# Kernel tuning notes

Measured on AMD Instinct MI355X. Metric: run time of the kernel, lower is better.

Reference implementation:

```python
import jax, jax.numpy as jnp
import numpy as np

N_NODES = 40000
N_EDGES = 400000
N_GRAPHS = 256
F_IN = 128
COND = 100
HEADS = 32
DIMS = [90, 45, 15, 5]
EPS = 1e-5


def setup_inputs() -> dict:
    key = jax.random.key(0)
    ks = iter(jax.random.split(key, 64))
    inp = {}
    inp["x"] = jax.random.normal(next(ks), (N_NODES, F_IN), dtype=jnp.float32)
    inp["edge_index"] = jax.random.randint(next(ks), (2, N_EDGES), 0, N_NODES, dtype=jnp.int32)
    inp["batch"] = jnp.sort(jax.random.randint(next(ks), (N_NODES,), 0, N_GRAPHS, dtype=jnp.int32))
    inp["conditional_features"] = jax.random.normal(next(ks), (COND,), dtype=jnp.float32)
    # GATConv params: W [in, H*C], a_src/a_dst [H, C], bias [C] (concat=False -> out is C)
    dims_in = [F_IN] + DIMS[:-1]
    for i, (ci, co) in enumerate(zip(dims_in, DIMS), start=1):
        sw = 1.0 / np.sqrt(ci)
        inp[f"W{i}"] = jax.random.normal(next(ks), (ci, HEADS * co), dtype=jnp.float32) * sw
        inp[f"as{i}"] = jax.random.normal(next(ks), (HEADS, co), dtype=jnp.float32) * (1.0 / np.sqrt(co))
        inp[f"ad{i}"] = jax.random.normal(next(ks), (HEADS, co), dtype=jnp.float32) * (1.0 / np.sqrt(co))
        inp[f"b{i}"] = jnp.zeros((co,), dtype=jnp.float32)
    # BatchNorm affine params (init gamma=1, beta=0) for sizes F_IN,90,45,15,5
    for i, c in enumerate([F_IN] + DIMS, start=1):
        inp[f"g{i}"] = jnp.ones((c,), dtype=jnp.float32)
        inp[f"be{i}"] = jnp.zeros((c,), dtype=jnp.float32)
    inp["fcW"] = jax.random.normal(next(ks), (DIMS[-1] + COND, 1), dtype=jnp.float32) * (1.0 / np.sqrt(DIMS[-1] + COND))
    inp["fcb"] = jnp.zeros((1,), dtype=jnp.float32)
    return inp


def _bn(x, g, b):
    # training-mode BatchNorm1d: batch statistics (biased var), eps=1e-5
    mu = x.mean(0)
    var = x.var(0)
    return g * (x - mu) * jax.lax.rsqrt(var + EPS) + b


def _gat(x, W, a_s, a_d, b, src, dst, n):
    H, C = a_s.shape
    h = (x @ W).reshape(n, H, C)                      # [N,H,C]
    s_src = jnp.einsum("nhc,hc->nh", h, a_s)
    s_dst = jnp.einsum("nhc,hc->nh", h, a_d)
    logit = jax.nn.leaky_relu(s_src[src] + s_dst[dst], 0.2)  # [E,H]
    m = jax.ops.segment_max(logit, dst, num_segments=n)
    e = jnp.exp(logit - m[dst])
    denom = jax.ops.segment_sum(e, dst, num_segments=n)
    alpha = e / denom[dst]                            # per-dst softmax, [E,H]
    out = jnp.zeros((n, C), dtype=x.dtype)
    for hi in range(H):  # fixed small loop over heads keeps peak memory at [E,C]
        out = out + jax.ops.segment_sum(alpha[:, hi, None] * h[src, hi, :], dst, num_segments=n)
    return out / H + b   # concat=False -> mean over heads, then bias


def reference(x, edge_index, batch, conditional_features,
              W1, as1, ad1, b1, W2, as2, ad2, b2, W3, as3, ad3, b3, W4, as4, ad4, b4,
              g1, be1, g2, be2, g3, be3, g4, be4, g5, be5, fcW, fcb):
    n = x.shape[0]
    loop = jnp.arange(n, dtype=edge_index.dtype)      # PyG GATConv adds self-loops by default
    src = jnp.concatenate([edge_index[0], loop])
    dst = jnp.concatenate([edge_index[1], loop])

    h = _bn(x, g1, be1)
    h = jax.nn.leaky_relu(_gat(h, W1, as1, ad1, b1, src, dst, n), 0.01)
    h = _bn(h, g2, be2)
    h = jax.nn.leaky_relu(_gat(h, W2, as2, ad2, b2, src, dst, n), 0.01)
    h = _bn(h, g3, be3)
    h = jax.nn.leaky_relu(_gat(h, W3, as3, ad3, b3, src, dst, n), 0.01)
    h = _bn(h, g4, be4)
    h = jax.nn.leaky_relu(_gat(h, W4, as4, ad4, b4, src, dst, n), 0.01)
    # dropout is identity in eval mode

    counts = jax.ops.segment_sum(jnp.ones((n,), dtype=h.dtype), batch, num_segments=N_GRAPHS)
    pooled = jax.ops.segment_sum(h, batch, num_segments=N_GRAPHS) / jnp.maximum(counts, 1.0)[:, None]
    z = jnp.concatenate([pooled, jnp.broadcast_to(conditional_features, (N_GRAPHS, COND))], axis=1)
    return jax.nn.sigmoid(z @ fcW + fcb).reshape(-1, 1)
```

## Files before the change

### kernel.cpp

```cpp
#include <hip/hip_runtime.h>
#include <hip/hip_bf16.h>

constexpr int NN = 40000;
constexpr int NE = 400000;
constexpr int NSLAB = 20000;
constexpr int MPAD = 20096;
constexpr int SCB = 256;
constexpr int SCHUNK = (NN + SCB - 1) / SCB;
constexpr int NPB = 512;

__device__ __forceinline__ unsigned short f2bf(float f) {
    unsigned int u = __float_as_uint(f);
    unsigned int r = (u + 0x7FFFu + ((u >> 16) & 1u)) >> 16;
    return (unsigned short)r;
}

__device__ __forceinline__ unsigned int cvt_pk_bf16(float a, float b) {
    unsigned int r;
    asm("v_cvt_pk_bf16_f32 %0, %1, %2" : "=v"(r) : "v"(a), "v"(b));
    return r;
}

__device__ __forceinline__ void load_lds16(const unsigned short* g, unsigned short* l) {
    __builtin_amdgcn_global_load_lds(
        (const __attribute__((address_space(1))) unsigned int*)(g),
        (__attribute__((address_space(3))) unsigned int*)(l), 16, 0, 0);
}

typedef __attribute__((ext_vector_type(8))) short bf16x8;
typedef __attribute__((ext_vector_type(4))) float f32x4;
typedef __attribute__((ext_vector_type(2))) float floatx2;

__global__ void bn_partial(const float* __restrict__ x, int N, int C,
                           float* __restrict__ partial) {
    int ch = threadIdx.x;
    if (ch >= C) return;
    float s = 0.f, sq = 0.f;
    for (int n = blockIdx.x; n < N; n += gridDim.x) {
        float v = x[(size_t)n * C + ch];
        s += v; sq += v * v;
    }
    partial[(size_t)blockIdx.x * 2 * C + ch]     = s;
    partial[(size_t)blockIdx.x * 2 * C + C + ch] = sq;
}

template <int CIN, int CP>
__global__ __launch_bounds__(256) void bn_apply_f(const float* __restrict__ x,
                                                  const float* __restrict__ partial,
                                                  const float* __restrict__ g,
                                                  const float* __restrict__ be,
                                                  float* __restrict__ scale_g,
                                                  float* __restrict__ shift_g,
                                                  unsigned short* __restrict__ xbn) {
    __shared__ float hs[2][128], hq[2][128];
    __shared__ float sc_l[CP], sh_l[CP];
    const int tid = threadIdx.x;
    const int half = tid >> 7, ch = tid & 127;
    if (ch < CIN) {
        float s = 0.f, sq = 0.f;
        for (int b = half * (NPB / 2); b < (half + 1) * (NPB / 2); ++b) {
            s  += partial[(size_t)b * 2 * CIN + ch];
            sq += partial[(size_t)b * 2 * CIN + CIN + ch];
        }
        hs[half][ch] = s; hq[half][ch] = sq;
    }
    __syncthreads();
    if (tid < CP) {
        float sc = 0.f, sh = 0.f;
        if (tid < CIN) {
            float s  = hs[0][tid] + hs[1][tid];
            float sq = hq[0][tid] + hq[1][tid];
            float mean = s / (float)NN;
            float var  = sq / (float)NN - mean * mean;
            float inv  = rsqrtf(var + 1e-5f);
            sc = g[tid] * inv;
            sh = be[tid] - mean * sc;
            if (blockIdx.x == 0) { scale_g[tid] = sc; shift_g[tid] = sh; }
        }
        sc_l[tid] = sc; sh_l[tid] = sh;
    }
    __syncthreads();
    const int total = NN * (CP / 2);
    for (int idx = blockIdx.x * 256 + tid; idx < total; idx += 256 * gridDim.x) {
        int n = idx / (CP / 2), c2 = idx % (CP / 2);
        int c = 2 * c2;
        float v0 = 0.f, v1 = 0.f;
        if (c < CIN)     v0 = sc_l[c] * x[(size_t)n * CIN + c] + sh_l[c];
        if (c + 1 < CIN) v1 = sc_l[c + 1] * x[(size_t)n * CIN + c + 1] + sh_l[c + 1];
        reinterpret_cast<unsigned int*>(xbn)[idx] = cvt_pk_bf16(v0, v1);
    }
}

struct PrepLayer {
    const float* W; const float* as_; const float* ad_;
    float* Wf; unsigned short* Wft; unsigned short* Wt;
    int CIN, CP, COUT, NP, bbase;
};
struct PrepArgs { PrepLayer L[4]; int nb; };

__global__ void prep_all(PrepArgs A) {
    int bid = blockIdx.x;
    int li = 0;
#pragma unroll
    for (int i = 1; i < 4; ++i)
        if (bid >= A.L[i].bbase) li = i;
    const PrepLayer& P = A.L[li];
    const int CIN = P.CIN, CP = P.CP, COUT = P.COUT;
    int b = bid - P.bbase;
    int tid = threadIdx.x;
    if (b < CP) {
        int cin = b;
        if (tid < 64) {
            int j = tid, h = j & 31;
            float s = 0.f;
            if (cin < CIN) {
                const float* a = (j < 32) ? P.as_ : P.ad_;
                const float* wrow = P.W + (size_t)cin * 32 * COUT + (size_t)h * COUT;
                const float* arow = a + (size_t)h * COUT;
                for (int c = 0; c < COUT; ++c) s += wrow[c] * arow[c];
            }
            P.Wf[cin * 64 + j] = s;
            P.Wft[j * CP + cin] = f2bf(s);
        }
    } else {
        int c = b - CP;
        for (int kk = tid; kk < 32 * CP; kk += blockDim.x) {
            int h = kk / CP, k = kk % CP;
            float v = 0.f;
            if (k < CIN && c < COUT)
                v = P.W[(size_t)k * (32 * COUT) + h * COUT + c] * (1.f / 32.f);
            P.Wt[(size_t)c * (32 * CP) + kk] = f2bf(v);
        }
    }
}

template <int CPK>
__global__ __launch_bounds__(256) void gemm_s(const unsigned short* __restrict__ xbn,
                                              const unsigned short* __restrict__ Wft,
                                              float* __restrict__ Sbuf) {
    constexpr int NC = CPK / 32;
    __shared__ unsigned short Ab[64 * 32];
    __shared__ unsigned short Bb[64 * 32];
    const int m0 = blockIdx.x * 64;
    const int tid = threadIdx.x;
    const int wv = tid >> 6, lane = tid & 63;
    const int mm = lane & 15, quad = lane >> 4;
    f32x4 acc[4];
#pragma unroll
    for (int t = 0; t < 4; ++t) acc[t] = f32x4{0.f, 0.f, 0.f, 0.f};

    for (int c = 0; c < NC; ++c) {
        int row = tid >> 2, gc = tid & 3;
        load_lds16(xbn + (size_t)(m0 + row) * CPK + c * 32 + gc * 8, Ab + (size_t)tid * 8);
        load_lds16(Wft + (size_t)row * CPK + c * 32 + gc * 8, Bb + (size_t)tid * 8);
        asm volatile("s_waitcnt vmcnt(0)" ::: "memory");
        __syncthreads();
        bf16x8 a = *reinterpret_cast<const bf16x8*>(&Ab[(wv * 16 + mm) * 32 + quad * 8]);
#pragma unroll
        for (int t = 0; t < 4; ++t) {
            bf16x8 b = *reinterpret_cast<const bf16x8*>(&Bb[(t * 16 + mm) * 32 + quad * 8]);
            acc[t] = __builtin_amdgcn_mfma_f32_16x16x32_bf16(a, b, acc[t], 0, 0, 0);
        }
        __syncthreads();
    }
    int rbase = m0 + wv * 16 + quad * 4;
#pragma unroll
    for (int t = 0; t < 4; ++t)
#pragma unroll
        for (int r = 0; r < 4; ++r)
            Sbuf[(size_t)(rbase + r) * 64 + t * 16 + mm] = acc[t][r];
}

__global__ __launch_bounds__(256) void gemm_bn(const float* __restrict__ X,
                                               const float* __restrict__ W,
                                               const float* __restrict__ scale,
                                               const float* __restrict__ shift,
                                               int Cin, int HC, float* __restrict__ OUT) {
    __shared__ float As[8][64];
    __shared__ float Bs[8][64];
    int tid = threadIdx.x;
    int n0 = blockIdx.y * 64;
    int j0 = blockIdx.x * 64;
    int tr = tid >> 4, tc = tid & 15;
    float acc[4][4] = {};
    for (int k0 = 0; k0 < Cin; k0 += 8) {
        int idx = tid;
#pragma unroll
        for (int it = 0; it < 2; ++it, idx += 256) {
            int row = idx >> 3, kk = idx & 7;
            int k = k0 + kk;
            float v = 0.f;
            if (k < Cin) v = scale[k] * X[(size_t)(n0 + row) * Cin + k] + shift[k];
            As[kk][row] = v;
        }
        int idx2 = tid;
#pragma unroll
        for (int it = 0; it < 2; ++it, idx2 += 256) {
            int col = idx2 & 63, kr = idx2 >> 6;
            int k = k0 + kr, j = j0 + col;
            float v = 0.f;
            if (k < Cin && j < HC) v = W[(size_t)k * HC + j];
            Bs[kr][col] = v;
        }
        __syncthreads();
#pragma unroll
        for (int kk = 0; kk < 8; ++kk) {
            float a[4], b[4];
#pragma unroll
            for (int i = 0; i < 4; ++i) a[i] = As[kk][tr * 4 + i];
#pragma unroll
            for (int j = 0; j < 4; ++j) b[j] = Bs[kk][tc * 4 + j];
#pragma unroll
            for (int i = 0; i < 4; ++i)
#pragma unroll
                for (int j = 0; j < 4; ++j) acc[i][j] += a[i] * b[j];
        }
        __syncthreads();
    }
#pragma unroll
    for (int i = 0; i < 4; ++i) {
        int row = n0 + tr * 4 + i;
#pragma unroll
        for (int j = 0; j < 4; ++j) {
            int col = j0 + tc * 4 + j;
            if (col < HC) OUT[(size_t)row * HC + col] = acc[i][j];
        }
    }
}

__global__ void deg_init(int* __restrict__ deg) {
    int n = blockIdx.x * blockDim.x + threadIdx.x;
    if (n < NN) deg[n] = 1;
}
__global__ void count_kernel(const int* __restrict__ dst, int* __restrict__ deg) {
    int e = blockIdx.x * blockDim.x + threadIdx.x;
    if (e < NE) atomicAdd(&deg[dst[e]], 1);
}
__global__ void scan_pass1(const int* __restrict__ deg, int* __restrict__ bsum) {
    __shared__ int red[256];
    int b = blockIdx.x, t = threadIdx.x;
    int lo = b * SCHUNK, hi = min(lo + SCHUNK, NN);
    int s = 0;
    for (int i = lo + t; i < hi; i += 256) s += deg[i];
    red[t] = s;
    __syncthreads();
    for (int off = 128; off > 0; off >>= 1) {
        if (t < off) red[t] += red[t + off];
        __syncthreads();
    }
    if (t == 0) bsum[b] = red[0];
}
__global__ void scan_pass2(const int* __restrict__ bsum, int* __restrict__ boff,
                           int* __restrict__ rowptr) {
    __shared__ int lds[256];
    int t = threadIdx.x;
    int v0 = bsum[t];
    lds[t] = v0;
    __syncthreads();
    for (int off = 1; off < 256; off <<= 1) {
        int v = (t >= off) ? lds[t - off] : 0;
        __syncthreads();
        lds[t] += v;
        __syncthreads();
    }
    boff[t] = lds[t] - v0;
    if (t == 255) rowptr[NN] = lds[255];
}
__global__ void scan_pass3(const int* __restrict__ deg, const int* __restrict__ boff,
                           int* __restrict__ rowptr, int* __restrict__ cursor) {
    __shared__ int lds[256];
    int b = blockIdx.x, t = threadIdx.x;
    int i = b * SCHUNK + t;
    int d = (t < SCHUNK && i < NN) ? deg[i] : 0;
    lds[t] = d;
    __syncthreads();
    for (int off = 1; off < 256; off <<= 1) {
        int v = (t >= off) ? lds[t - off] : 0;
        __syncthreads();
        lds[t] += v;
        __syncthreads();
    }
    if (t < SCHUNK && i < NN) {
        int excl = lds[t] - d + boff[b];
        rowptr[i] = excl;
        cursor[i] = excl;
    }
}
__global__ void scatter_all(const int* __restrict__ src, const int* __restrict__ dst,
                            int* __restrict__ cursor, int* __restrict__ colsrc) {
    int e = blockIdx.x * blockDim.x + threadIdx.x;
    if (e < NE) {
        int pos = atomicAdd(&cursor[dst[e]], 1);
        colsrc[pos] = src[e];
    } else if (e < NE + NN) {
        int n = e - NE;
        int pos = atomicAdd(&cursor[n], 1);
        colsrc[pos] = n;
    }
}

template <int CIN, int CP>
__global__ __launch_bounds__(256) void agg_x(const unsigned short* __restrict__ xbn,
                                             const float* __restrict__ S,
                                             const int* __restrict__ rowptr,
                                             const int* __restrict__ colsrc,
                                             int n0, unsigned short* __restrict__ z) {
    constexpr int BS = 256, CH = 32, J = CP / 8;
    constexpr bool V4 = (J % 4 == 0);
    constexpr int NACC = V4 ? (J / 4) : (J / 2);
    __shared__ __align__(16) float x_lds[CH * CP];
    __shared__ float w_lds[CH * 32];
    __shared__ int cs_lds[CH];
    __shared__ float red_m[8][32];
    __shared__ float red_s[8][32];

    int n = n0 + blockIdx.x;
    int tid = threadIdx.x;
    int start = rowptr[n], end = rowptr[n + 1];
    const int h = tid & 31, g = tid >> 5;
    const int cbase = g * J;
    const float sd = S[(size_t)n * 64 + 32 + h];

    float m_reg = -INFINITY, d_reg = 0.f;
    f32x4 acc4[V4 ? NACC : 1];
    floatx2 acc2[V4 ? 1 : NACC];
    if constexpr (V4) {
#pragma unroll
        for (int j = 0; j < NACC; ++j) acc4[j] = f32x4{0.f, 0.f, 0.f, 0.f};
    } else {
#pragma unroll
        for (int j = 0; j < NACC; ++j) acc2[j] = floatx2{0.f, 0.f};
    }

    for (int chunk = start; chunk < end; chunk += CH) {
        int ce = min(CH, end - chunk);
        int ce32 = ce * 32;
        if (tid < 32 && tid < ce) cs_lds[tid] = colsrc[chunk + tid];
        __syncthreads();

        float lreg[4];
        float pmx = -INFINITY;
#pragma unroll
        for (int p = 0; p < 4; ++p) {
            int idx = p * 256 + tid;
            lreg[p] = -INFINITY;
            if (idx < ce32) {
                int e = idx >> 5;
                float l = S[(size_t)cs_lds[e] * 64 + h] + sd;
                l = l > 0.f ? l : 0.2f * l;
                lreg[p] = l;
                pmx = fmaxf(pmx, l);
            }
        }
        red_m[g][h] = pmx;
        for (int idx = tid; idx < ce * (CP / 4); idx += BS) {
            int e = idx / (CP / 4), c4 = idx % (CP / 4);
            uint2 u = reinterpret_cast<const uint2*>(xbn)[(size_t)cs_lds[e] * (CP / 4) + c4];
            f32x4 t;
            t[0] = __uint_as_float(u.x << 16);
            t[1] = __uint_as_float(u.x & 0xFFFF0000u);
            t[2] = __uint_as_float(u.y << 16);
            t[3] = __uint_as_float(u.y & 0xFFFF0000u);
            *reinterpret_cast<f32x4*>(&x_lds[e * CP + 4 * c4]) = t;
        }
        __syncthreads();

        float cm = red_m[0][h];
#pragma unroll
        for (int s2 = 1; s2 < 8; ++s2) cm = fmaxf(cm, red_m[s2][h]);
        float newm = fmaxf(m_reg, cm);
        float r = (m_reg == -INFINITY) ? 0.f : __expf(m_reg - newm);
        m_reg = newm;

        float ps = 0.f;
#pragma unroll
        for (int p = 0; p < 4; ++p) {
            int idx = p * 256 + tid;
            if (idx < ce32) {
                float v = __expf(lreg[p] - m_reg);
                w_lds[idx] = v;
                ps += v;
            }
        }
        red_s[g][h] = ps;
        __syncthreads();

        float ss = red_s[0][h];
#pragma unroll
        for (int s2 = 1; s2 < 8; ++s2) ss += red_s[s2][h];
        d_reg = d_reg * r + ss;

        if constexpr (V4) {
            f32x4 rr4 = {r, r, r, r};
#pragma unroll
            for (int j = 0; j < NACC; ++j) acc4[j] *= rr4;
            for (int e = 0; e < ce; ++e) {
                float w = w_lds[e * 32 + h];
                f32x4 w4 = {w, w, w, w};
                const f32x4* xv = reinterpret_cast<const f32x4*>(&x_lds[e * CP + cbase]);
#pragma unroll
                for (int j = 0; j < NACC; ++j) acc4[j] += w4 * xv[j];
            }
        } else {
            floatx2 rr2 = {r, r};
#pragma unroll
            for (int j = 0; j < NACC; ++j) acc2[j] *= rr2;
            for (int e = 0; e < ce; ++e) {
                float w = w_lds[e * 32 + h];
                floatx2 w2 = {w, w};
                const floatx2* xv = reinterpret_cast<const floatx2*>(&x_lds[e * CP + cbase]);
#pragma unroll
                for (int j = 0; j < NACC; ++j) acc2[j] += w2 * xv[j];
            }
        }
    }

    float dinv = 1.f / d_reg;
    if constexpr (V4) {
        uint2* zp = reinterpret_cast<uint2*>(
            z + (size_t)(n - n0) * (32 * CP) + h * CP + cbase);
#pragma unroll
        for (int j = 0; j < NACC; ++j) {
            uint2 t;
            t.x = cvt_pk_bf16(acc4[j][0] * dinv, acc4[j][1] * dinv);
            t.y = cvt_pk_bf16(acc4[j][2] * dinv, acc4[j][3] * dinv);
            zp[j] = t;
        }
    } else {
        unsigned int* zp = reinterpret_cast<unsigned int*>(
            z + (size_t)(n - n0) * (32 * CP) + h * CP + cbase);
#pragma unroll
        for (int j = 0; j < NACC; ++j)
            zp[j] = cvt_pk_bf16(acc2[j][0] * dinv, acc2[j][1] * dinv);
    }
}

template <int NT, int KP, int KS, bool FB>
__global__ __launch_bounds__(256) void gemm_z_t(const unsigned short* __restrict__ z,
                                                const unsigned short* __restrict__ Wt,
                                                float* __restrict__ obuf,
                                                const float* __restrict__ bias,
                                                int n0, int COUT) {
    constexpr int NP = NT * 16;
    constexpr int KSEG = KP / KS;
    constexpr int NC = KSEG / 64;
    constexpr int MT = 128;
    __shared__ unsigned short Abuf[2][MT * 64];
    __shared__ unsigned short Bbuf[2][NP * 64];

    const int m0 = blockIdx.x * MT;
    const int kbeg = blockIdx.y * KSEG;
    const int tid = threadIdx.x;
    const int wv = tid >> 6;
    const int lane = tid & 63;
    const int mm = lane & 15, quad = lane >> 4;

    auto stage = [&](int buf, int kk) {
#pragma unroll
        for (int it = 0; it < 4; ++it) {
            int gi = it * 256 + tid;
            int row = gi >> 3, gc = gi & 7;
            int srow = m0 + row;
            if (srow > NSLAB - 1) srow = NSLAB - 1;
            const unsigned short* src = z + (size_t)srow * KP + kk + gc * 8;
            unsigned short* dst = &Abuf[buf][(size_t)(it * 256 + wv * 64) * 8];
            load_lds16(src, dst);
        }
#pragma unroll
        for (int it = 0; it < (NP * 8 + 255) / 256; ++it) {
            int gi = it * 256 + tid;
            if (gi < NP * 8) {
                int row = gi >> 3, gc = gi & 7;
                const unsigned short* src = Wt + (size_t)row * KP + kk + gc * 8;
                unsigned short* dst = &Bbuf[buf][(size_t)(it * 256 + wv * 64) * 8];
                load_lds16(src, dst);
            }
        }
    };

    f32x4 acc[2][NT];
#pragma unroll
    for (int f = 0; f < 2; ++f)
#pragma unroll
        for (int t = 0; t < NT; ++t) acc[f][t] = f32x4{0.f, 0.f, 0.f, 0.f};

    stage(0, kbeg);
    for (int c = 0; c < NC; ++c) {
        asm volatile("s_waitcnt vmcnt(0)" ::: "memory");
        __syncthreads();
        int cur = c & 1;
        if (c + 1 < NC) stage(cur ^ 1, kbeg + (c + 1) * 64);
        const unsigned short* Ab = Abuf[cur];
        const unsigned short* Bb = Bbuf[cur];
#pragma unroll
        for (int hh = 0; hh < 2; ++hh) {
            bf16x8 a0 = *reinterpret_cast<const bf16x8*>(&Ab[(wv * 32 + mm) * 64 + hh * 32 + quad * 8]);
            bf16x8 a1 = *reinterpret_cast<const bf16x8*>(&Ab[(wv * 32 + 16 + mm) * 64 + hh * 32 + quad * 8]);
#pragma unroll
            for (int t = 0; t < NT; ++t) {
                bf16x8 b = *reinterpret_cast<const bf16x8*>(&Bb[(t * 16 + mm) * 64 + hh * 32 + quad * 8]);
                acc[0][t] = __builtin_amdgcn_mfma_f32_16x16x32_bf16(a0, b, acc[0][t], 0, 0, 0);
                acc[1][t] = __builtin_amdgcn_mfma_f32_16x16x32_bf16(a1, b, acc[1][t], 0, 0, 0);
            }
        }
        __syncthreads();
    }

    int row0 = quad * 4;
    if constexpr (FB) {
#pragma unroll
        for (int f = 0; f < 2; ++f) {
#pragma unroll
            for (int t = 0; t < NT; ++t) {
                int cc = t * 16 + mm;
#pragma unroll
                for (int r = 0; r < 4; ++r) {
                    int m = m0 + wv * 32 + f * 16 + row0 + r;
                    if (m < NSLAB && cc < COUT) {
                        float v = acc[f][t][r] + bias[cc];
                        v = v > 0.f ? v : 0.01f * v;
                        obuf[(size_t)(n0 + m) * COUT + cc] = v;
                    }
                }
            }
        }
    } else {
        float* pb = obuf + (size_t)blockIdx.y * MPAD * NP;
#pragma unroll
        for (int f = 0; f < 2; ++f) {
#pragma unroll
            for (int t = 0; t < NT; ++t) {
                int cc = t * 16 + mm;
#pragma unroll
                for (int r = 0; r < 4; ++r) {
                    int m = m0 + wv * 32 + f * 16 + row0 + r;
                    pb[(size_t)m * NP + cc] = acc[f][t][r];
                }
            }
        }
    }
}

__global__ void reduce_parts(const float* __restrict__ pbuf, int KS, int NPAD, int COUT,
                             const float* __restrict__ bias, int n0,
                             float* __restrict__ xout) {
    int idx = blockIdx.x * blockDim.x + threadIdx.x;
    if (idx >= NSLAB * NPAD) return;
    int m = idx / NPAD, c = idx % NPAD;
    if (c >= COUT) return;
    float s = 0.f;
    for (int p = 0; p < KS; ++p) s += pbuf[(size_t)p * MPAD * NPAD + (size_t)m * NPAD + c];
    float v = s + bias[c];
    v = v > 0.f ? v : 0.01f * v;
    xout[(size_t)(n0 + m) * COUT + c] = v;
}

__global__ __launch_bounds__(64) void pool_head(const float* __restrict__ x4,
                                                const int* __restrict__ batch,
                                                const float* __restrict__ cond,
                                                const float* __restrict__ fcW,
                                                const float* __restrict__ fcb,
                                                float* __restrict__ out) {
    int g = blockIdx.x;
    int lane = threadIdx.x;
    int lo = 0, hi = NN;
    while (lo < hi) { int mid = (lo + hi) >> 1; if (batch[mid] < g) lo = mid + 1; else hi = mid; }
    int lo2 = lo, hi2 = NN;
    while (lo2 < hi2) { int mid = (lo2 + hi2) >> 1; if (batch[mid] < g + 1) lo2 = mid + 1; else hi2 = mid; }
    int beg = lo, end = lo2;

    float s[5] = {0.f, 0.f, 0.f, 0.f, 0.f};
    for (int n = beg + lane; n < end; n += 64) {
#pragma unroll
        for (int c = 0; c < 5; ++c) s[c] += x4[(size_t)n * 5 + c];
    }
    float cz = 0.f;
    if (lane < 100) cz = cond[lane] * fcW[5 + lane];
    if (lane + 64 < 100) cz += cond[lane + 64] * fcW[5 + lane + 64];
#pragma unroll
    for (int off = 32; off > 0; off >>= 1) {
#pragma unroll
        for (int c = 0; c < 5; ++c) s[c] += __shfl_down(s[c], off, 64);
        cz += __shfl_down(cz, off, 64);
    }
    if (lane == 0) {
        float cnt = fmaxf((float)(end - beg), 1.f);
        float zv = fcb[0] + cz;
#pragma unroll
        for (int c = 0; c < 5; ++c) zv += (s[c] / cnt) * fcW[c];
        out[g] = 1.f / (1.f + __expf(-zv));
    }
}

struct LayerBufs {
    float* partial; float* scale; float* shift;
    unsigned short* xbn; unsigned short* zbuf;
    float* Sbuf; float* pbuf; const int* rowptr; const int* colsrc;
};

template <int CIN, int CP, int COUT, int NP, int NT, int KS>
static void run_layer(const float* xin, const float* Wf, const unsigned short* Wft,
                      const unsigned short* Wt,
                      const float* Bv, const float* G, const float* Be,
                      float* xout, const LayerBufs& B, hipStream_t stream) {
    constexpr int KP = 32 * CP;
    constexpr int NPAD = NT * 16;
    bn_partial<<<NPB, 128, 0, stream>>>(xin, NN, CIN, B.partial);
    bn_apply_f<CIN, CP><<<512, 256, 0, stream>>>(xin, B.partial, G, Be,
                                                 B.scale, B.shift, B.xbn);
    if constexpr (CP >= 64) {
        gemm_s<CP><<<NN / 64, 256, 0, stream>>>(B.xbn, Wft, B.Sbuf);
    } else {
        gemm_bn<<<dim3(1, NN / 64), 256, 0, stream>>>(xin, Wf, B.scale, B.shift, CIN, 64, B.Sbuf);
    }
    for (int s = 0; s < 2; ++s) {
        int n0 = s * NSLAB;
        agg_x<CIN, CP><<<NSLAB, 256, 0, stream>>>(B.xbn, B.Sbuf, B.rowptr, B.colsrc, n0, B.zbuf);
        if constexpr (KS > 1) {
            gemm_z_t<NT, KP, KS, false><<<dim3(MPAD / 128, KS), 256, 0, stream>>>(
                B.zbuf, Wt, B.pbuf, nullptr, n0, COUT);
            reduce_parts<<<(NSLAB * NPAD + 255) / 256, 256, 0, stream>>>(
                B.pbuf, KS, NPAD, COUT, Bv, n0, xout);
        } else {
            gemm_z_t<NT, KP, 1, true><<<dim3(MPAD / 128, 1), 256, 0, stream>>>(
                B.zbuf, Wt, xout, Bv, n0, COUT);
        }
    }
}

extern "C" void kernel_launch(void* const* d_in, const int* in_sizes, int n_in,
                              void* d_out, int out_size, void* d_ws, size_t ws_size,
                              hipStream_t stream) {
    (void)in_sizes; (void)n_in; (void)out_size;
    const float* x     = (const float*)d_in[0];
    const int*   ei    = (const int*)d_in[1];
    const int*   batch = (const int*)d_in[2];
    const float* cond  = (const float*)d_in[3];
    const float* W[4]  = {(const float*)d_in[4],  (const float*)d_in[8],
                          (const float*)d_in[12], (const float*)d_in[16]};
    const float* Asp[4] = {(const float*)d_in[5],  (const float*)d_in[9],
                           (const float*)d_in[13], (const float*)d_in[17]};
    const float* Adp[4] = {(const float*)d_in[6],  (const float*)d_in[10],
                           (const float*)d_in[14], (const float*)d_in[18]};
    const float* Bv[4]  = {(const float*)d_in[7],  (const float*)d_in[11],
                           (const float*)d_in[15], (const float*)d_in[19]};
    const float* G[4]   = {(const float*)d_in[20], (const float*)d_in[22],
                           (const float*)d_in[24], (const float*)d_in[26]};
    const float* Be[4]  = {(const float*)d_in[21], (const float*)d_in[23],
                           (const float*)d_in[25], (const float*)d_in[27]};
    const float* fcW = (const float*)d_in[30];
    const float* fcb = (const float*)d_in[31];
    float* out = (float*)d_out;

    char* base = (char*)d_ws;
    size_t off = 0;
    auto alloc = [&](size_t b) {
        size_t o = off;
        off += (b + 255) & ~(size_t)255;
        return (void*)(base + o);
    };
    unsigned short* zbuf = (unsigned short*)alloc((size_t)NSLAB * 4096 * 2);
    unsigned short* xbn  = (unsigned short*)alloc((size_t)NN * 128 * 2);
    float* pbuf    = (float*)alloc((size_t)4 * MPAD * 96 * 4);
    float* xbuf    = (float*)alloc((size_t)NN * 90 * 4);
    float* Sbuf    = (float*)alloc((size_t)NN * 64 * 4);
    float* partial = (float*)alloc((size_t)NPB * 2 * 128 * 4);
    float* scale   = (float*)alloc(128 * 4);
    float* shift   = (float*)alloc(128 * 4);
    const int CPs[4]  = {128, 96, 48, 16};
    const int NPs[4]  = {96, 48, 16, 16};
    const int CINs[4] = {128, 90, 45, 15};
    const int COUTs[4] = {90, 45, 15, 5};
    float* Wf_a[4]; unsigned short* Wft_a[4]; unsigned short* Wt_a[4];
    for (int i = 0; i < 4; ++i) {
        Wf_a[i]  = (float*)alloc((size_t)CPs[i] * 64 * 4);
        Wft_a[i] = (unsigned short*)alloc((size_t)64 * CPs[i] * 2);
        Wt_a[i]  = (unsigned short*)alloc((size_t)NPs[i] * 32 * CPs[i] * 2);
    }
    int* deg     = (int*)alloc((size_t)NN * 4);
    int* rowptr  = (int*)alloc((size_t)(NN + 1) * 4);
    int* cursor  = (int*)alloc((size_t)NN * 4);
    int* colsrc  = (int*)alloc((size_t)(NE + NN) * 4);
    int* bsum    = (int*)alloc((size_t)SCB * 4);
    int* boff    = (int*)alloc((size_t)SCB * 4);
    if (off > ws_size) return;

    const int* srcp = ei;
    const int* dstp = ei + NE;

    PrepArgs PA;
    int bb = 0;
    for (int i = 0; i < 4; ++i) {
        PA.L[i] = PrepLayer{W[i], Asp[i], Adp[i], Wf_a[i], Wft_a[i], Wt_a[i],
                            CINs[i], CPs[i], COUTs[i], NPs[i], bb};
        bb += CPs[i] + NPs[i];
    }
    PA.nb = bb;
    prep_all<<<bb, 256, 0, stream>>>(PA);

    deg_init<<<(NN + 255) / 256, 256, 0, stream>>>(deg);
    count_kernel<<<(NE + 255) / 256, 256, 0, stream>>>(dstp, deg);
    scan_pass1<<<SCB, 256, 0, stream>>>(deg, bsum);
    scan_pass2<<<1, 256, 0, stream>>>(bsum, boff, rowptr);
    scan_pass3<<<SCB, 256, 0, stream>>>(deg, boff, rowptr, cursor);
    scatter_all<<<(NE + NN + 255) / 256, 256, 0, stream>>>(srcp, dstp, cursor, colsrc);

    LayerBufs B{partial, scale, shift, xbn, zbuf, Sbuf, pbuf, rowptr, colsrc};

    run_layer<128, 128, 90, 96, 6, 4>(x,    Wf_a[0], Wft_a[0], Wt_a[0], Bv[0], G[0], Be[0], xbuf, B, stream);
    run_layer< 90,  96, 45, 48, 3, 3>(xbuf, Wf_a[1], Wft_a[1], Wt_a[1], Bv[1], G[1], Be[1], xbuf, B, stream);
    run_layer< 45,  48, 15, 16, 1, 1>(xbuf, Wf_a[2], Wft_a[2], Wt_a[2], Bv[2], G[2], Be[2], xbuf, B, stream);
    run_layer< 15,  16,  5, 16, 1, 1>(xbuf, Wf_a[3], Wft_a[3], Wt_a[3], Bv[3], G[3], Be[3], xbuf, B, stream);

    pool_head<<<256, 64, 0, stream>>>(xbuf, batch, cond, fcW, fcb, out);
}
```

Before: 1.043 ms.

## Shrink aggregation chunk and GEMM M-tile, replace degree init with memset

The edge chunk in agg_x drops from 32 to 16, which halves the LDS footprint and register arrays. That should let more blocks fit per CU, though it adds more chunk iterations and syncs for high-degree nodes. The z-GEMM M tile drops from 128 to 64 rows, so each wave handles one 16-row fragment and twice as many blocks launch, giving more parallelism at the cost of less reuse of the B tile. The deg_init kernel is replaced by hipMemsetAsync, and the self-loop +1 is folded into the scan passes.

```diff
diff --git a/kernel.cpp b/kernel.cpp
--- a/kernel.cpp
+++ b/kernel.cpp
@@ -228,10 +228,6 @@
     }
 }
 
-__global__ void deg_init(int* __restrict__ deg) {
-    int n = blockIdx.x * blockDim.x + threadIdx.x;
-    if (n < NN) deg[n] = 1;
-}
 __global__ void count_kernel(const int* __restrict__ dst, int* __restrict__ deg) {
     int e = blockIdx.x * blockDim.x + threadIdx.x;
     if (e < NE) atomicAdd(&deg[dst[e]], 1);
@@ -241,7 +237,7 @@
     int b = blockIdx.x, t = threadIdx.x;
     int lo = b * SCHUNK, hi = min(lo + SCHUNK, NN);
     int s = 0;
-    for (int i = lo + t; i < hi; i += 256) s += deg[i];
+    for (int i = lo + t; i < hi; i += 256) s += deg[i] + 1;
     red[t] = s;
     __syncthreads();
     for (int off = 128; off > 0; off >>= 1) {
@@ -271,7 +267,7 @@
     __shared__ int lds[256];
     int b = blockIdx.x, t = threadIdx.x;
     int i = b * SCHUNK + t;
-    int d = (t < SCHUNK && i < NN) ? deg[i] : 0;
+    int d = (t < SCHUNK && i < NN) ? (deg[i] + 1) : 0;
     lds[t] = d;
     __syncthreads();
     for (int off = 1; off < 256; off <<= 1) {
@@ -305,9 +301,10 @@
                                              const int* __restrict__ rowptr,
                                              const int* __restrict__ colsrc,
                                              int n0, unsigned short* __restrict__ z) {
-    constexpr int BS = 256, CH = 32, J = CP / 8;
+    constexpr int BS = 256, CH = 16, J = CP / 8;
     constexpr bool V4 = (J % 4 == 0);
     constexpr int NACC = V4 ? (J / 4) : (J / 2);
+    constexpr int LIT = CH * 32 / 256;
     __shared__ __align__(16) float x_lds[CH * CP];
     __shared__ float w_lds[CH * 32];
     __shared__ int cs_lds[CH];
@@ -335,13 +332,13 @@
     for (int chunk = start; chunk < end; chunk += CH) {
         int ce = min(CH, end - chunk);
         int ce32 = ce * 32;
-        if (tid < 32 && tid < ce) cs_lds[tid] = colsrc[chunk + tid];
-        __syncthreads();
-
-        float lreg[4];
+        if (tid < CH && tid < ce) cs_lds[tid] = colsrc[chunk + tid];
+        __syncthreads();
+
+        float lreg[LIT];
         float pmx = -INFINITY;
 #pragma unroll
-        for (int p = 0; p < 4; ++p) {
+        for (int p = 0; p < LIT; ++p) {
             int idx = p * 256 + tid;
             lreg[p] = -INFINITY;
             if (idx < ce32) {
@@ -374,7 +371,7 @@
 
         float ps = 0.f;
 #pragma unroll
-        for (int p = 0; p < 4; ++p) {
+        for (int p = 0; p < LIT; ++p) {
             int idx = p * 256 + tid;
             if (idx < ce32) {
                 float v = __expf(lreg[p] - m_reg);
@@ -444,7 +441,7 @@
     constexpr int NP = NT * 16;
     constexpr int KSEG = KP / KS;
     constexpr int NC = KSEG / 64;
-    constexpr int MT = 128;
+    constexpr int MT = 64;
     __shared__ unsigned short Abuf[2][MT * 64];
     __shared__ unsigned short Bbuf[2][NP * 64];
 
@@ -457,7 +454,7 @@
 
     auto stage = [&](int buf, int kk) {
 #pragma unroll
-        for (int it = 0; it < 4; ++it) {
+        for (int it = 0; it < 2; ++it) {
             int gi = it * 256 + tid;
             int row = gi >> 3, gc = gi & 7;
             int srow = m0 + row;
@@ -478,11 +475,9 @@
         }
     };
 
-    f32x4 acc[2][NT];
-#pragma unroll
-    for (int f = 0; f < 2; ++f)
-#pragma unroll
-        for (int t = 0; t < NT; ++t) acc[f][t] = f32x4{0.f, 0.f, 0.f, 0.f};
+    f32x4 acc[NT];
+#pragma unroll
+    for (int t = 0; t < NT; ++t) acc[t] = f32x4{0.f, 0.f, 0.f, 0.f};
 
     stage(0, kbeg);
     for (int c = 0; c < NC; ++c) {
@@ -494,13 +489,11 @@
         const unsigned short* Bb = Bbuf[cur];
 #pragma unroll
         for (int hh = 0; hh < 2; ++hh) {
-            bf16x8 a0 = *reinterpret_cast<const bf16x8*>(&Ab[(wv * 32 + mm) * 64 + hh * 32 + quad * 8]);
-            bf16x8 a1 = *reinterpret_cast<const bf16x8*>(&Ab[(wv * 32 + 16 + mm) * 64 + hh * 32 + quad * 8]);
+            bf16x8 a0 = *reinterpret_cast<const bf16x8*>(&Ab[(wv * 16 + mm) * 64 + hh * 32 + quad * 8]);
 #pragma unroll
             for (int t = 0; t < NT; ++t) {
                 bf16x8 b = *reinterpret_cast<const bf16x8*>(&Bb[(t * 16 + mm) * 64 + hh * 32 + quad * 8]);
-                acc[0][t] = __builtin_amdgcn_mfma_f32_16x16x32_bf16(a0, b, acc[0][t], 0, 0, 0);
-                acc[1][t] = __builtin_amdgcn_mfma_f32_16x16x32_bf16(a1, b, acc[1][t], 0, 0, 0);
+                acc[t] = __builtin_amdgcn_mfma_f32_16x16x32_bf16(a0, b, acc[t], 0, 0, 0);
             }
         }
         __syncthreads();
@@ -509,33 +502,27 @@
     int row0 = quad * 4;
     if constexpr (FB) {
 #pragma unroll
-        for (int f = 0; f < 2; ++f) {
-#pragma unroll
-            for (int t = 0; t < NT; ++t) {
-                int cc = t * 16 + mm;
-#pragma unroll
-                for (int r = 0; r < 4; ++r) {
-                    int m = m0 + wv * 32 + f * 16 + row0 + r;
-                    if (m < NSLAB && cc < COUT) {
-                        float v = acc[f][t][r] + bias[cc];
-                        v = v > 0.f ? v : 0.01f * v;
-                        obuf[(size_t)(n0 + m) * COUT + cc] = v;
-                    }
+        for (int t = 0; t < NT; ++t) {
+            int cc = t * 16 + mm;
+#pragma unroll
+            for (int r = 0; r < 4; ++r) {
+                int m = m0 + wv * 16 + row0 + r;
+                if (m < NSLAB && cc < COUT) {
+                    float v = acc[t][r] + bias[cc];
+                    v = v > 0.f ? v : 0.01f * v;
+                    obuf[(size_t)(n0 + m) * COUT + cc] = v;
                 }
             }
         }
     } else {
         float* pb = obuf + (size_t)blockIdx.y * MPAD * NP;
 #pragma unroll
-        for (int f = 0; f < 2; ++f) {
-#pragma unroll
-            for (int t = 0; t < NT; ++t) {
-                int cc = t * 16 + mm;
-#pragma unroll
-                for (int r = 0; r < 4; ++r) {
-                    int m = m0 + wv * 32 + f * 16 + row0 + r;
-                    pb[(size_t)m * NP + cc] = acc[f][t][r];
-                }
+        for (int t = 0; t < NT; ++t) {
+            int cc = t * 16 + mm;
+#pragma unroll
+            for (int r = 0; r < 4; ++r) {
+                int m = m0 + wv * 16 + row0 + r;
+                pb[(size_t)m * NP + cc] = acc[t][r];
             }
         }
     }
@@ -617,12 +604,12 @@
         int n0 = s * NSLAB;
         agg_x<CIN, CP><<<NSLAB, 256, 0, stream>>>(B.xbn, B.Sbuf, B.rowptr, B.colsrc, n0, B.zbuf);
         if constexpr (KS > 1) {
-            gemm_z_t<NT, KP, KS, false><<<dim3(MPAD / 128, KS), 256, 0, stream>>>(
+            gemm_z_t<NT, KP, KS, false><<<dim3(MPAD / 64, KS), 256, 0, stream>>>(
                 B.zbuf, Wt, B.pbuf, nullptr, n0, COUT);
             reduce_parts<<<(NSLAB * NPAD + 255) / 256, 256, 0, stream>>>(
                 B.pbuf, KS, NPAD, COUT, Bv, n0, xout);
         } else {
-            gemm_z_t<NT, KP, 1, true><<<dim3(MPAD / 128, 1), 256, 0, stream>>>(
+            gemm_z_t<NT, KP, 1, true><<<dim3(MPAD / 64, 1), 256, 0, stream>>>(
                 B.zbuf, Wt, xout, Bv, n0, COUT);
         }
     }
@@ -698,7 +685,7 @@
     PA.nb = bb;
     prep_all<<<bb, 256, 0, stream>>>(PA);
 
-    deg_init<<<(NN + 255) / 256, 256, 0, stream>>>(deg);
+    hipMemsetAsync(deg, 0, (size_t)NN * 4, stream);
     count_kernel<<<(NE + 255) / 256, 256, 0, stream>>>(dstp, deg);
     scan_pass1<<<SCB, 256, 0, stream>>>(deg, bsum);
     scan_pass2<<<1, 256, 0, stream>>>(bsum, boff, rowptr);
```

New measurement: 1.018 ms (median of 2 runs). 2.4% less time.
